# Performance work log

Measured on AMD Instinct MI355X. Metric: run time of the kernel, lower is better.

The kernel has to match this reference:

```python
import jax, jax.numpy as jnp
import numpy as np
import math

TWO_PI = 2.0 * math.pi
LN_EPS = 1e-5


def _phase(pos_f, d):
    # periods[i, j] = i * d + j + 2 ; phi[s, i, j] = cos(2*pi*k_s / periods[i, j])
    i = jnp.arange(d, dtype=jnp.float32)
    periods = i[:, None] * d + i[None, :] + 2.0  # (d, d)
    return jnp.cos(TWO_PI * pos_f[:, None, None] / periods)  # (S, d, d)


def _layernorm(x, g, b):
    mu = jnp.mean(x, axis=-1, keepdims=True)
    var = jnp.mean(jnp.square(x - mu), axis=-1, keepdims=True)
    return (x - mu) * jax.lax.rsqrt(var + LN_EPS) * g + b


def _pos_nk(x, P, phi):
    # Nk[b, s, i] = sum_j P[i, j] * x[b, s, j] * phi[s, i, j]
    return jnp.einsum('bsj,ij,sij->bsi', x, P, phi)


def setup_inputs() -> dict:
    key = jax.random.key(0)
    ks = jax.random.split(key, 10)
    B, S, V, D = 4, 4096, 64, 128
    NTOK = 64  # 4^3 k-mer tokens
    u = lambda k, shp, a: jax.random.uniform(k, shp, jnp.float32, -a, a)
    return {
        'tokens': jax.random.randint(ks[0], (B, S), 0, NTOK, dtype=jnp.int32),
        'positions': jnp.arange(S, dtype=jnp.int32),
        'emb': jax.random.normal(ks[1], (NTOK, V), jnp.float32),
        'char_P': u(ks[2], (V, V), 0.1),
        'M1': u(ks[3], (D, V), 0.5),
        'P1': u(ks[4], (D, D), 0.1),
        'g1': jnp.ones((D,), jnp.float32),
        'b1': jnp.zeros((D,), jnp.float32),
        'R1': u(ks[5], (D, V), 0.1),
        'M2': u(ks[6], (D, D), 0.5),
        'P2': u(ks[7], (D, D), 0.1),
        'g2': jnp.ones((D,), jnp.float32),
        'b2': jnp.zeros((D,), jnp.float32),
    }


def reference(tokens, positions, emb, char_P, M1, P1, g1, b1, R1, M2, P2, g2, b2):
    pos_f = positions.astype(jnp.float32)
    V, D1, D2 = emb.shape[1], M1.shape[0], M2.shape[0]
    # char level (Layer 0): embedding + position-modulated mixing
    x = emb[tokens]                               # (B, S, V)
    h = _pos_nk(x, char_P, _phase(pos_f, V))      # (B, S, V)
    # Layer 1: separate residual (in_dim != out_dim -> linear proj)
    t1 = jnp.einsum('bsj,ij->bsi', h, M1)         # (B, S, D1)
    n1 = _pos_nk(_layernorm(t1, g1, b1), P1, _phase(pos_f, D1))
    h1 = n1 + jnp.einsum('bsj,ij->bsi', h, R1)
    # Layer 2: shared residual (residual = x @ M.T, pre-norm)
    t2 = jnp.einsum('bsj,ij->bsi', h1, M2)        # (B, S, D2)
    n2 = _pos_nk(_layernorm(t2, g2, b2), P2, _phase(pos_f, D2))
    return n2 + t2
```

## Files before the change

kernel.cpp:

```cpp
#include <hip/hip_runtime.h>

typedef unsigned short u16;
typedef unsigned int   u32;
typedef float f32x2 __attribute__((ext_vector_type(2)));

#define BB 4
#define SS 4096
#define VV 64
#define DD 128

#define CPT_OFF 0
#define M1T_OFF 4096
#define R1T_OFF 12288
#define P1T_OFF 20480
#define M2T_OFF 36864
#define P2T_OFF 53248
#define EMB_OFF 69632
#define G1_OFF  73728
#define B1_OFF  73856
#define G2_OFF  73984
#define B2_OFF  74112
#define WS_F32_WEIGHTS 74240

__device__ __forceinline__ float bf2f(u16 u) {
    return __uint_as_float(((u32)u) << 16);
}
__device__ __forceinline__ float ldany(const void* p, int idx, bool f32) {
    return f32 ? ((const float*)p)[idx] : bf2f(((const u16*)p)[idx]);
}
__device__ __forceinline__ float phase_cos(float pos, float pf) {
    float x = pos * __builtin_amdgcn_rcpf(pf);
    float r = __builtin_amdgcn_fractf(x);
    return __builtin_amdgcn_cosf(r);
}
__device__ __forceinline__ float f4get(float4 v, int i) {
    return i == 0 ? v.x : i == 1 ? v.y : i == 2 ? v.z : v.w;
}
struct acc2x2 {
    f32x2 lo, hi;
    __device__ __forceinline__ void zero() { lo = (f32x2)0.f; hi = (f32x2)0.f; }
    __device__ __forceinline__ void fma(float s, float4 v) {
        f32x2 s2 = {s, s};
        f32x2 vlo = {v.x, v.y}, vhi = {v.z, v.w};
        lo = __builtin_elementwise_fma(s2, vlo, lo);
        hi = __builtin_elementwise_fma(s2, vhi, hi);
    }
    __device__ __forceinline__ float get(int b) const {
        return b == 0 ? lo[0] : b == 1 ? lo[1] : b == 2 ? hi[0] : hi[1];
    }
};

__global__ void prep_ws(const void* __restrict__ cP,  const void* __restrict__ M1,
                        const void* __restrict__ R1,  const void* __restrict__ P1,
                        const void* __restrict__ M2,  const void* __restrict__ P2,
                        const void* __restrict__ emb, const void* __restrict__ g1,
                        const void* __restrict__ b1,  const void* __restrict__ g2,
                        const void* __restrict__ b2,  float* __restrict__ wsf)
{
    const bool f32 = (((const u32*)g1)[0] == 0x3F800000u);
    const int m = blockIdx.x;
    const int t = threadIdx.x;
    if (m == 17) {
        for (int idx = t; idx < 4608; idx += 256) {
            float v; int dst;
            if (idx < 4096) { v = ldany(emb, idx, f32); dst = EMB_OFF + idx; }
            else {
                int off = idx - 4096, which = off >> 7, e = off & 127;
                const void* p = (which == 0) ? g1 : (which == 1) ? b1
                              : (which == 2) ? g2 : b2;
                v = ldany(p, e, f32);
                dst = G1_OFF + which * 128 + e;
            }
            wsf[dst] = v;
        }
        return;
    }
    __shared__ float tile[64][65];
    const void* src; int doff, R, C, ti0, tj0;
    if (m == 0)      { src = cP; doff = CPT_OFF; R = 64;  C = 64;  ti0 = 0;            tj0 = 0; }
    else if (m <= 2) { src = M1; doff = M1T_OFF; R = 128; C = 64;  ti0 = (m - 1) * 64; tj0 = 0; }
    else if (m <= 4) { src = R1; doff = R1T_OFF; R = 128; C = 64;  ti0 = (m - 3) * 64; tj0 = 0; }
    else {
        const int k = m - 5, w = k >> 2, q = k & 3;
        src  = (w == 0) ? P1 : (w == 1) ? M2 : P2;
        doff = (w == 0) ? P1T_OFF : (w == 1) ? M2T_OFF : P2T_OFF;
        R = 128; C = 128; ti0 = (q >> 1) * 64; tj0 = (q & 1) * 64;
    }
    float* dst = wsf + doff;
    #pragma unroll
    for (int k = 0; k < 16; ++k) {
        int idx = k * 256 + t;
        int i = idx >> 6, j = idx & 63;
        tile[i][j] = ldany(src, (ti0 + i) * C + (tj0 + j), f32);
    }
    __syncthreads();
    #pragma unroll
    for (int k = 0; k < 16; ++k) {
        int idx = k * 256 + t;
        int j = idx >> 6, i = idx & 63;
        int gj = tj0 + j, gi = ti0 + i;
        dst[((gj >> 2) * R + gi) * 4 + (gj & 3)] = tile[i][j];
    }
}

template<bool WS>
__global__ void __launch_bounds__(256, 4)
fused_hier(const int* __restrict__ tokens,
           const int* __restrict__ positions,
           const void* __restrict__ emb,
           const void* __restrict__ cP,
           const void* __restrict__ M1,
           const void* __restrict__ P1,
           const void* __restrict__ g1,
           const void* __restrict__ b1,
           const void* __restrict__ R1,
           const void* __restrict__ M2,
           const void* __restrict__ P2,
           const void* __restrict__ g2,
           const void* __restrict__ b2,
           const float* __restrict__ wsf,
           float* __restrict__ out)
{
    __shared__ float4 x4v[VV];
    __shared__ float4 h4v[VV];
    __shared__ float4 lnv[DD];
    __shared__ float4 h1v[DD];
    __shared__ float  t14p[4 * DD];
    __shared__ float  t2p[4 * DD];
    __shared__ float  partp[2048];

    float* x4  = (float*)x4v;
    float* h4  = (float*)h4v;
    float* lnf = (float*)lnv;
    float* h1f = (float*)h1v;

    const int t = threadIdx.x;
    const int s = blockIdx.x;
    if (s >= SS) return;
    const bool f32 = WS ? true : (((const u32*)g1)[0] == 0x3F800000u);
    const float pos = (float)positions[s];
    const int i6 = t & 63,  q4 = t >> 6;
    const int i7 = t & 127, h2 = t >> 7;
    const int w  = t >> 6,  l  = t & 63;

    {
        int tok = tokens[q4 * SS + s];
        float v = WS ? wsf[EMB_OFF + tok * VV + i6] : ldany(emb, tok * VV + i6, f32);
        x4[i6 * 4 + q4] = v;
    }
    __syncthreads();

    {
        acc2x2 a; a.zero();
        const int jb = q4 * 16;
        float pf = (float)(i6 * VV + jb + 2);
        #pragma unroll
        for (int q = 0; q < 4; ++q) {
            const int jg = q4 * 4 + q;
            float4 w4;
            if (WS) w4 = *(const float4*)&wsf[CPT_OFF + (jg * VV + i6) * 4];
            #pragma unroll
            for (int k = 0; k < 4; ++k) {
                const int j = jb + q * 4 + k;
                float c  = phase_cos(pos, pf);
                float wt = (WS ? f4get(w4, k) : ldany(cP, i6 * VV + j, f32)) * c;
                a.fma(wt, x4v[j]);
                pf += 1.0f;
            }
        }
        #pragma unroll
        for (int b = 0; b < 4; ++b)
            partp[b * 256 + q4 * 64 + i6] = a.get(b);
    }
    __syncthreads();

    {
        float hv = partp[q4 * 256 + i6]       + partp[q4 * 256 + 64 + i6]
                 + partp[q4 * 256 + 128 + i6] + partp[q4 * 256 + 192 + i6];
        h4[i6 * 4 + q4] = hv;
    }
    __syncthreads();

    {
        acc2x2 at, ar; at.zero(); ar.zero();
        #pragma unroll
        for (int q = 0; q < 8; ++q) {
            const int jg = h2 * 8 + q;
            float4 m4, r4;
            if (WS) {
                m4 = *(const float4*)&wsf[M1T_OFF + (jg * DD + i7) * 4];
                r4 = *(const float4*)&wsf[R1T_OFF + (jg * DD + i7) * 4];
            }
            #pragma unroll
            for (int k = 0; k < 4; ++k) {
                const int j = h2 * 32 + q * 4 + k;
                float mv = WS ? f4get(m4, k) : ldany(M1, i7 * VV + j, f32);
                float rv = WS ? f4get(r4, k) : ldany(R1, i7 * VV + j, f32);
                float4 hb = h4v[j];
                at.fma(mv, hb);
                ar.fma(rv, hb);
            }
        }
        #pragma unroll
        for (int b = 0; b < 4; ++b) {
            partp[b * 256 + h2 * 128 + i7]        = at.get(b);
            partp[1024 + b * 256 + h2 * 128 + i7] = ar.get(b);
        }
    }
    __syncthreads();

    float res0, res1;
    {
        const int b0 = h2 * 2, b1 = b0 + 1;
        t14p[b0 * 128 + i7] = partp[b0 * 256 + i7] + partp[b0 * 256 + 128 + i7];
        t14p[b1 * 128 + i7] = partp[b1 * 256 + i7] + partp[b1 * 256 + 128 + i7];
        res0 = partp[1024 + b0 * 256 + i7] + partp[1024 + b0 * 256 + 128 + i7];
        res1 = partp[1024 + b1 * 256 + i7] + partp[1024 + b1 * 256 + 128 + i7];
    }
    __syncthreads();

    {
        float v0 = t14p[w * 128 + l], v1 = t14p[w * 128 + 64 + l];
        float s1 = v0 + v1;
        #pragma unroll
        for (int m = 1; m < 64; m <<= 1) s1 += __shfl_xor(s1, m, 64);
        float mu = s1 * (1.0f / 128.0f);
        float d0 = v0 - mu, d1 = v1 - mu;
        float s2 = d0 * d0 + d1 * d1;
        #pragma unroll
        for (int m = 1; m < 64; m <<= 1) s2 += __shfl_xor(s2, m, 64);
        float rs = rsqrtf(s2 * (1.0f / 128.0f) + 1e-5f);
        float ga = WS ? wsf[G1_OFF + l]      : ldany(g1, l, f32);
        float gb = WS ? wsf[G1_OFF + l + 64] : ldany(g1, l + 64, f32);
        float ba = WS ? wsf[B1_OFF + l]      : ldany(b1, l, f32);
        float bb = WS ? wsf[B1_OFF + l + 64] : ldany(b1, l + 64, f32);
        lnf[l * 4 + w]        = d0 * rs * ga + ba;
        lnf[(l + 64) * 4 + w] = d1 * rs * gb + bb;
    }
    __syncthreads();

    {
        acc2x2 acc; acc.zero();
        float pf = (float)(i7 * DD + h2 * 64 + 2);
        #pragma unroll
        for (int q = 0; q < 16; ++q) {
            const int jg = h2 * 16 + q;
            float4 w4;
            if (WS) w4 = *(const float4*)&wsf[P1T_OFF + (jg * DD + i7) * 4];
            #pragma unroll
            for (int k = 0; k < 4; ++k) {
                const int j = h2 * 64 + q * 4 + k;
                float c = phase_cos(pos, pf);
                float wt = (WS ? f4get(w4, k) : ldany(P1, i7 * DD + j, f32)) * c;
                acc.fma(wt, lnv[j]);
                pf += 1.0f;
            }
        }
        #pragma unroll
        for (int b = 0; b < 4; ++b)
            partp[b * 256 + h2 * 128 + i7] = acc.get(b);
    }
    __syncthreads();

    {
        const int b0 = h2 * 2, b1 = b0 + 1;
        h1f[i7 * 4 + b0] = res0 + partp[b0 * 256 + i7] + partp[b0 * 256 + 128 + i7];
        h1f[i7 * 4 + b1] = res1 + partp[b1 * 256 + i7] + partp[b1 * 256 + 128 + i7];
    }
    __syncthreads();

    {
        acc2x2 acc; acc.zero();
        #pragma unroll
        for (int q = 0; q < 16; ++q) {
            const int jg = h2 * 16 + q;
            float4 m4;
            if (WS) m4 = *(const float4*)&wsf[M2T_OFF + (jg * DD + i7) * 4];
            #pragma unroll
            for (int k = 0; k < 4; ++k) {
                const int j = h2 * 64 + q * 4 + k;
                float mv = WS ? f4get(m4, k) : ldany(M2, i7 * DD + j, f32);
                acc.fma(mv, h1v[j]);
            }
        }
        #pragma unroll
        for (int b = 0; b < 4; ++b)
            partp[b * 256 + h2 * 128 + i7] = acc.get(b);
    }
    __syncthreads();

    {
        const int b0 = h2 * 2, b1 = b0 + 1;
        t2p[b0 * 128 + i7] = partp[b0 * 256 + i7] + partp[b0 * 256 + 128 + i7];
        t2p[b1 * 128 + i7] = partp[b1 * 256 + i7] + partp[b1 * 256 + 128 + i7];
    }
    __syncthreads();

    {
        float v0 = t2p[w * 128 + l], v1 = t2p[w * 128 + 64 + l];
        float s1 = v0 + v1;
        #pragma unroll
        for (int m = 1; m < 64; m <<= 1) s1 += __shfl_xor(s1, m, 64);
        float mu = s1 * (1.0f / 128.0f);
        float d0 = v0 - mu, d1 = v1 - mu;
        float s2 = d0 * d0 + d1 * d1;
        #pragma unroll
        for (int m = 1; m < 64; m <<= 1) s2 += __shfl_xor(s2, m, 64);
        float rs = rsqrtf(s2 * (1.0f / 128.0f) + 1e-5f);
        float ga = WS ? wsf[G2_OFF + l]      : ldany(g2, l, f32);
        float gb = WS ? wsf[G2_OFF + l + 64] : ldany(g2, l + 64, f32);
        float ba = WS ? wsf[B2_OFF + l]      : ldany(b2, l, f32);
        float bb = WS ? wsf[B2_OFF + l + 64] : ldany(b2, l + 64, f32);
        lnf[l * 4 + w]        = d0 * rs * ga + ba;
        lnf[(l + 64) * 4 + w] = d1 * rs * gb + bb;
    }
    __syncthreads();

    {
        acc2x2 acc; acc.zero();
        float pf = (float)(i7 * DD + h2 * 64 + 2);
        #pragma unroll
        for (int q = 0; q < 16; ++q) {
            const int jg = h2 * 16 + q;
            float4 w4;
            if (WS) w4 = *(const float4*)&wsf[P2T_OFF + (jg * DD + i7) * 4];
            #pragma unroll
            for (int k = 0; k < 4; ++k) {
                const int j = h2 * 64 + q * 4 + k;
                float c = phase_cos(pos, pf);
                float wt = (WS ? f4get(w4, k) : ldany(P2, i7 * DD + j, f32)) * c;
                acc.fma(wt, lnv[j]);
                pf += 1.0f;
            }
        }
        #pragma unroll
        for (int b = 0; b < 4; ++b)
            partp[b * 256 + h2 * 128 + i7] = acc.get(b);
    }
    __syncthreads();

    {
        const int b0 = h2 * 2, b1 = b0 + 1;
        float v0 = partp[b0 * 256 + i7] + partp[b0 * 256 + 128 + i7] + t2p[b0 * 128 + i7];
        float v1 = partp[b1 * 256 + i7] + partp[b1 * 256 + 128 + i7] + t2p[b1 * 128 + i7];
        out[(b0 * SS + s) * DD + i7] = v0;
        out[(b1 * SS + s) * DD + i7] = v1;
    }
}

extern "C" void kernel_launch(void* const* d_in, const int* in_sizes, int n_in,
                              void* d_out, int out_size, void* d_ws, size_t ws_size,
                              hipStream_t stream)
{
    const int* tokens    = (const int*)d_in[0];
    const int* positions = (const int*)d_in[1];
    const void* emb = d_in[2];
    const void* cP  = d_in[3];
    const void* M1  = d_in[4];
    const void* P1  = d_in[5];
    const void* g1  = d_in[6];
    const void* b1  = d_in[7];
    const void* R1  = d_in[8];
    const void* M2  = d_in[9];
    const void* P2  = d_in[10];
    const void* g2  = d_in[11];
    const void* b2  = d_in[12];
    float* out = (float*)d_out;
    float* wsf = (float*)d_ws;

    const bool tw = (ws_size >= (size_t)WS_F32_WEIGHTS * sizeof(float));
    if (tw) {
        prep_ws<<<18, 256, 0, stream>>>(cP, M1, R1, P1, M2, P2, emb,
                                        g1, b1, g2, b2, wsf);
        fused_hier<true><<<SS, 256, 0, stream>>>(tokens, positions, emb, cP, M1, P1,
                                                 g1, b1, R1, M2, P2, g2, b2, wsf, out);
    } else {
        fused_hier<false><<<SS, 256, 0, stream>>>(tokens, positions, emb, cP, M1, P1,
                                                  g1, b1, R1, M2, P2, g2, b2, wsf, out);
    }
}
```

Baseline: 144.8 us.

## Process two sequence positions per block to reuse weight loads and reciprocals

```diff
diff --git a/kernel.cpp b/kernel.cpp
--- a/kernel.cpp
+++ b/kernel.cpp
@@ -28,10 +28,8 @@
 __device__ __forceinline__ float ldany(const void* p, int idx, bool f32) {
     return f32 ? ((const float*)p)[idx] : bf2f(((const u16*)p)[idx]);
 }
-__device__ __forceinline__ float phase_cos(float pos, float pf) {
-    float x = pos * __builtin_amdgcn_rcpf(pf);
-    float r = __builtin_amdgcn_fractf(x);
-    return __builtin_amdgcn_cosf(r);
+__device__ __forceinline__ float cos_rev(float pos, float rcpv) {
+    return __builtin_amdgcn_cosf(__builtin_amdgcn_fractf(pos * rcpv));
 }
 __device__ __forceinline__ float f4get(float4 v, int i) {
     return i == 0 ? v.x : i == 1 ? v.y : i == 2 ? v.z : v.w;
@@ -104,7 +102,7 @@
 }
 
 template<bool WS>
-__global__ void __launch_bounds__(256, 4)
+__global__ void __launch_bounds__(256, 2)
 fused_hier(const int* __restrict__ tokens,
            const int* __restrict__ positions,
            const void* __restrict__ emb,
@@ -121,13 +119,13 @@
            const float* __restrict__ wsf,
            float* __restrict__ out)
 {
-    __shared__ float4 x4v[VV];
-    __shared__ float4 h4v[VV];
-    __shared__ float4 lnv[DD];
-    __shared__ float4 h1v[DD];
-    __shared__ float  t14p[4 * DD];
-    __shared__ float  t2p[4 * DD];
-    __shared__ float  partp[2048];
+    __shared__ float4 x4v[2 * VV];
+    __shared__ float4 h4v[2 * VV];
+    __shared__ float4 lnv[2 * DD];
+    __shared__ float4 h1v[2 * DD];
+    __shared__ float  t14p[2 * 4 * DD];
+    __shared__ float  t2p[2 * 4 * DD];
+    __shared__ float  partp[2 * 2048];
 
     float* x4  = (float*)x4v;
     float* h4  = (float*)h4v;
@@ -135,23 +133,28 @@
     float* h1f = (float*)h1v;
 
     const int t = threadIdx.x;
-    const int s = blockIdx.x;
-    if (s >= SS) return;
+    const int s0 = blockIdx.x;
+    if (s0 >= SS / 2) return;
+    const int s1 = s0 + SS / 2;
     const bool f32 = WS ? true : (((const u32*)g1)[0] == 0x3F800000u);
-    const float pos = (float)positions[s];
+    const float pos0 = (float)positions[s0];
+    const float pos1 = (float)positions[s1];
     const int i6 = t & 63,  q4 = t >> 6;
     const int i7 = t & 127, h2 = t >> 7;
     const int w  = t >> 6,  l  = t & 63;
 
     {
-        int tok = tokens[q4 * SS + s];
-        float v = WS ? wsf[EMB_OFF + tok * VV + i6] : ldany(emb, tok * VV + i6, f32);
-        x4[i6 * 4 + q4] = v;
-    }
-    __syncthreads();
-
-    {
-        acc2x2 a; a.zero();
+        int tk0 = tokens[q4 * SS + s0];
+        int tk1 = tokens[q4 * SS + s1];
+        float v0 = WS ? wsf[EMB_OFF + tk0 * VV + i6] : ldany(emb, tk0 * VV + i6, f32);
+        float v1 = WS ? wsf[EMB_OFF + tk1 * VV + i6] : ldany(emb, tk1 * VV + i6, f32);
+        x4[i6 * 4 + q4]       = v0;
+        x4[256 + i6 * 4 + q4] = v1;
+    }
+    __syncthreads();
+
+    {
+        acc2x2 a0, a1; a0.zero(); a1.zero();
         const int jb = q4 * 16;
         float pf = (float)(i6 * VV + jb + 2);
         #pragma unroll
@@ -162,85 +165,116 @@
             #pragma unroll
             for (int k = 0; k < 4; ++k) {
                 const int j = jb + q * 4 + k;
-                float c  = phase_cos(pos, pf);
-                float wt = (WS ? f4get(w4, k) : ldany(cP, i6 * VV + j, f32)) * c;
-                a.fma(wt, x4v[j]);
+                float rcpv = __builtin_amdgcn_rcpf(pf);
+                float wv = WS ? f4get(w4, k) : ldany(cP, i6 * VV + j, f32);
+                a0.fma(wv * cos_rev(pos0, rcpv), x4v[j]);
+                a1.fma(wv * cos_rev(pos1, rcpv), x4v[64 + j]);
                 pf += 1.0f;
             }
         }
         #pragma unroll
-        for (int b = 0; b < 4; ++b)
-            partp[b * 256 + q4 * 64 + i6] = a.get(b);
-    }
-    __syncthreads();
-
-    {
-        float hv = partp[q4 * 256 + i6]       + partp[q4 * 256 + 64 + i6]
-                 + partp[q4 * 256 + 128 + i6] + partp[q4 * 256 + 192 + i6];
-        h4[i6 * 4 + q4] = hv;
-    }
-    __syncthreads();
-
-    {
-        acc2x2 at, ar; at.zero(); ar.zero();
+        for (int b = 0; b < 4; ++b) {
+            partp[b * 256 + q4 * 64 + i6]        = a0.get(b);
+            partp[2048 + b * 256 + q4 * 64 + i6] = a1.get(b);
+        }
+    }
+    __syncthreads();
+
+    {
+        #pragma unroll
+        for (int p = 0; p < 2; ++p) {
+            const int o = p * 2048;
+            float hv = partp[o + q4 * 256 + i6]       + partp[o + q4 * 256 + 64 + i6]
+                     + partp[o + q4 * 256 + 128 + i6] + partp[o + q4 * 256 + 192 + i6];
+            h4[p * 256 + i6 * 4 + q4] = hv;
+        }
+    }
+    __syncthreads();
+
+    {
+        acc2x2 at0, at1; at0.zero(); at1.zero();
         #pragma unroll
         for (int q = 0; q < 8; ++q) {
             const int jg = h2 * 8 + q;
-            float4 m4, r4;
-            if (WS) {
-                m4 = *(const float4*)&wsf[M1T_OFF + (jg * DD + i7) * 4];
-                r4 = *(const float4*)&wsf[R1T_OFF + (jg * DD + i7) * 4];
-            }
+            float4 m4;
+            if (WS) m4 = *(const float4*)&wsf[M1T_OFF + (jg * DD + i7) * 4];
             #pragma unroll
             for (int k = 0; k < 4; ++k) {
                 const int j = h2 * 32 + q * 4 + k;
                 float mv = WS ? f4get(m4, k) : ldany(M1, i7 * VV + j, f32);
+                at0.fma(mv, h4v[j]);
+                at1.fma(mv, h4v[64 + j]);
+            }
+        }
+        #pragma unroll
+        for (int b = 0; b < 4; ++b) {
+            partp[b * 256 + h2 * 128 + i7]        = at0.get(b);
+            partp[2048 + b * 256 + h2 * 128 + i7] = at1.get(b);
+        }
+    }
+    {
+        acc2x2 ar0, ar1; ar0.zero(); ar1.zero();
+        #pragma unroll
+        for (int q = 0; q < 8; ++q) {
+            const int jg = h2 * 8 + q;
+            float4 r4;
+            if (WS) r4 = *(const float4*)&wsf[R1T_OFF + (jg * DD + i7) * 4];
+            #pragma unroll
+            for (int k = 0; k < 4; ++k) {
+                const int j = h2 * 32 + q * 4 + k;
                 float rv = WS ? f4get(r4, k) : ldany(R1, i7 * VV + j, f32);
-                float4 hb = h4v[j];
-                at.fma(mv, hb);
-                ar.fma(rv, hb);
-            }
-        }
-        #pragma unroll
-        for (int b = 0; b < 4; ++b) {
-            partp[b * 256 + h2 * 128 + i7]        = at.get(b);
-            partp[1024 + b * 256 + h2 * 128 + i7] = ar.get(b);
-        }
-    }
-    __syncthreads();
-
-    float res0, res1;
+                ar0.fma(rv, h4v[j]);
+                ar1.fma(rv, h4v[64 + j]);
+            }
+        }
+        #pragma unroll
+        for (int b = 0; b < 4; ++b) {
+            partp[1024 + b * 256 + h2 * 128 + i7]        = ar0.get(b);
+            partp[2048 + 1024 + b * 256 + h2 * 128 + i7] = ar1.get(b);
+        }
+    }
+    __syncthreads();
+
+    float res[2][2];
     {
         const int b0 = h2 * 2, b1 = b0 + 1;
-        t14p[b0 * 128 + i7] = partp[b0 * 256 + i7] + partp[b0 * 256 + 128 + i7];
-        t14p[b1 * 128 + i7] = partp[b1 * 256 + i7] + partp[b1 * 256 + 128 + i7];
-        res0 = partp[1024 + b0 * 256 + i7] + partp[1024 + b0 * 256 + 128 + i7];
-        res1 = partp[1024 + b1 * 256 + i7] + partp[1024 + b1 * 256 + 128 + i7];
-    }
-    __syncthreads();
-
-    {
-        float v0 = t14p[w * 128 + l], v1 = t14p[w * 128 + 64 + l];
-        float s1 = v0 + v1;
-        #pragma unroll
-        for (int m = 1; m < 64; m <<= 1) s1 += __shfl_xor(s1, m, 64);
-        float mu = s1 * (1.0f / 128.0f);
-        float d0 = v0 - mu, d1 = v1 - mu;
-        float s2 = d0 * d0 + d1 * d1;
-        #pragma unroll
-        for (int m = 1; m < 64; m <<= 1) s2 += __shfl_xor(s2, m, 64);
-        float rs = rsqrtf(s2 * (1.0f / 128.0f) + 1e-5f);
+        #pragma unroll
+        for (int p = 0; p < 2; ++p) {
+            const int o = p * 2048, to = p * 512;
+            t14p[to + b0 * 128 + i7] = partp[o + b0 * 256 + i7] + partp[o + b0 * 256 + 128 + i7];
+            t14p[to + b1 * 128 + i7] = partp[o + b1 * 256 + i7] + partp[o + b1 * 256 + 128 + i7];
+            res[p][0] = partp[o + 1024 + b0 * 256 + i7] + partp[o + 1024 + b0 * 256 + 128 + i7];
+            res[p][1] = partp[o + 1024 + b1 * 256 + i7] + partp[o + 1024 + b1 * 256 + 128 + i7];
+        }
+    }
+    __syncthreads();
+
+    {
         float ga = WS ? wsf[G1_OFF + l]      : ldany(g1, l, f32);
         float gb = WS ? wsf[G1_OFF + l + 64] : ldany(g1, l + 64, f32);
         float ba = WS ? wsf[B1_OFF + l]      : ldany(b1, l, f32);
         float bb = WS ? wsf[B1_OFF + l + 64] : ldany(b1, l + 64, f32);
-        lnf[l * 4 + w]        = d0 * rs * ga + ba;
-        lnf[(l + 64) * 4 + w] = d1 * rs * gb + bb;
-    }
-    __syncthreads();
-
-    {
-        acc2x2 acc; acc.zero();
+        #pragma unroll
+        for (int p = 0; p < 2; ++p) {
+            const int to = p * 512;
+            float v0 = t14p[to + w * 128 + l], v1 = t14p[to + w * 128 + 64 + l];
+            float s1 = v0 + v1;
+            #pragma unroll
+            for (int m = 1; m < 64; m <<= 1) s1 += __shfl_xor(s1, m, 64);
+            float mu = s1 * (1.0f / 128.0f);
+            float d0 = v0 - mu, d1 = v1 - mu;
+            float s2 = d0 * d0 + d1 * d1;
+            #pragma unroll
+            for (int m = 1; m < 64; m <<= 1) s2 += __shfl_xor(s2, m, 64);
+            float rs = rsqrtf(s2 * (1.0f / 128.0f) + 1e-5f);
+            lnf[p * 512 + l * 4 + w]        = d0 * rs * ga + ba;
+            lnf[p * 512 + (l + 64) * 4 + w] = d1 * rs * gb + bb;
+        }
+    }
+    __syncthreads();
+
+    {
+        acc2x2 a0, a1; a0.zero(); a1.zero();
         float pf = (float)(i7 * DD + h2 * 64 + 2);
         #pragma unroll
         for (int q = 0; q < 16; ++q) {
@@ -250,27 +284,34 @@
             #pragma unroll
             for (int k = 0; k < 4; ++k) {
                 const int j = h2 * 64 + q * 4 + k;
-                float c = phase_cos(pos, pf);
-                float wt = (WS ? f4get(w4, k) : ldany(P1, i7 * DD + j, f32)) * c;
-                acc.fma(wt, lnv[j]);
+                float rcpv = __builtin_amdgcn_rcpf(pf);
+                float wv = WS ? f4get(w4, k) : ldany(P1, i7 * DD + j, f32);
+                a0.fma(wv * cos_rev(pos0, rcpv), lnv[j]);
+                a1.fma(wv * cos_rev(pos1, rcpv), lnv[128 + j]);
                 pf += 1.0f;
             }
         }
         #pragma unroll
-        for (int b = 0; b < 4; ++b)
-            partp[b * 256 + h2 * 128 + i7] = acc.get(b);
+        for (int b = 0; b < 4; ++b) {
+            partp[b * 256 + h2 * 128 + i7]        = a0.get(b);
+            partp[2048 + b * 256 + h2 * 128 + i7] = a1.get(b);
+        }
     }
     __syncthreads();
 
     {
         const int b0 = h2 * 2, b1 = b0 + 1;
-        h1f[i7 * 4 + b0] = res0 + partp[b0 * 256 + i7] + partp[b0 * 256 + 128 + i7];
-        h1f[i7 * 4 + b1] = res1 + partp[b1 * 256 + i7] + partp[b1 * 256 + 128 + i7];
-    }
-    __syncthreads();
-
-    {
-        acc2x2 acc; acc.zero();
+        #pragma unroll
+        for (int p = 0; p < 2; ++p) {
+            const int o = p * 2048;
+            h1f[p * 512 + i7 * 4 + b0] = res[p][0] + partp[o + b0 * 256 + i7] + partp[o + b0 * 256 + 128 + i7];
+            h1f[p * 512 + i7 * 4 + b1] = res[p][1] + partp[o + b1 * 256 + i7] + partp[o + b1 * 256 + 128 + i7];
+        }
+    }
+    __syncthreads();
+
+    {
+        acc2x2 a0, a1; a0.zero(); a1.zero();
         #pragma unroll
         for (int q = 0; q < 16; ++q) {
             const int jg = h2 * 16 + q;
@@ -280,44 +321,55 @@
             for (int k = 0; k < 4; ++k) {
                 const int j = h2 * 64 + q * 4 + k;
                 float mv = WS ? f4get(m4, k) : ldany(M2, i7 * DD + j, f32);
-                acc.fma(mv, h1v[j]);
-            }
-        }
-        #pragma unroll
-        for (int b = 0; b < 4; ++b)
-            partp[b * 256 + h2 * 128 + i7] = acc.get(b);
+                a0.fma(mv, h1v[j]);
+                a1.fma(mv, h1v[128 + j]);
+            }
+        }
+        #pragma unroll
+        for (int b = 0; b < 4; ++b) {
+            partp[b * 256 + h2 * 128 + i7]        = a0.get(b);
+            partp[2048 + b * 256 + h2 * 128 + i7] = a1.get(b);
+        }
     }
     __syncthreads();
 
     {
         const int b0 = h2 * 2, b1 = b0 + 1;
-        t2p[b0 * 128 + i7] = partp[b0 * 256 + i7] + partp[b0 * 256 + 128 + i7];
-        t2p[b1 * 128 + i7] = partp[b1 * 256 + i7] + partp[b1 * 256 + 128 + i7];
-    }
-    __syncthreads();
-
-    {
-        float v0 = t2p[w * 128 + l], v1 = t2p[w * 128 + 64 + l];
-        float s1 = v0 + v1;
-        #pragma unroll
-        for (int m = 1; m < 64; m <<= 1) s1 += __shfl_xor(s1, m, 64);
-        float mu = s1 * (1.0f / 128.0f);
-        float d0 = v0 - mu, d1 = v1 - mu;
-        float s2 = d0 * d0 + d1 * d1;
-        #pragma unroll
-        for (int m = 1; m < 64; m <<= 1) s2 += __shfl_xor(s2, m, 64);
-        float rs = rsqrtf(s2 * (1.0f / 128.0f) + 1e-5f);
+        #pragma unroll
+        for (int p = 0; p < 2; ++p) {
+            const int o = p * 2048, to = p * 512;
+            t2p[to + b0 * 128 + i7] = partp[o + b0 * 256 + i7] + partp[o + b0 * 256 + 128 + i7];
+            t2p[to + b1 * 128 + i7] = partp[o + b1 * 256 + i7] + partp[o + b1 * 256 + 128 + i7];
+        }
+    }
+    __syncthreads();
+
+    {
         float ga = WS ? wsf[G2_OFF + l]      : ldany(g2, l, f32);
         float gb = WS ? wsf[G2_OFF + l + 64] : ldany(g2, l + 64, f32);
         float ba = WS ? wsf[B2_OFF + l]      : ldany(b2, l, f32);
         float bb = WS ? wsf[B2_OFF + l + 64] : ldany(b2, l + 64, f32);
-        lnf[l * 4 + w]        = d0 * rs * ga + ba;
-        lnf[(l + 64) * 4 + w] = d1 * rs * gb + bb;
-    }
-    __syncthreads();
-
-    {
-        acc2x2 acc; acc.zero();
+        #pragma unroll
+        for (int p = 0; p < 2; ++p) {
+            const int to = p * 512;
+            float v0 = t2p[to + w * 128 + l], v1 = t2p[to + w * 128 + 64 + l];
+            float s1 = v0 + v1;
+            #pragma unroll
+            for (int m = 1; m < 64; m <<= 1) s1 += __shfl_xor(s1, m, 64);
+            float mu = s1 * (1.0f / 128.0f);
+            float d0 = v0 - mu, d1 = v1 - mu;
+            float s2 = d0 * d0 + d1 * d1;
+            #pragma unroll
+            for (int m = 1; m < 64; m <<= 1) s2 += __shfl_xor(s2, m, 64);
+            float rs = rsqrtf(s2 * (1.0f / 128.0f) + 1e-5f);
+            lnf[p * 512 + l * 4 + w]        = d0 * rs * ga + ba;
+            lnf[p * 512 + (l + 64) * 4 + w] = d1 * rs * gb + bb;
+        }
+    }
+    __syncthreads();
+
+    {
+        acc2x2 a0, a1; a0.zero(); a1.zero();
         float pf = (float)(i7 * DD + h2 * 64 + 2);
         #pragma unroll
         for (int q = 0; q < 16; ++q) {
@@ -327,24 +379,32 @@
             #pragma unroll
             for (int k = 0; k < 4; ++k) {
                 const int j = h2 * 64 + q * 4 + k;
-                float c = phase_cos(pos, pf);
-                float wt = (WS ? f4get(w4, k) : ldany(P2, i7 * DD + j, f32)) * c;
-                acc.fma(wt, lnv[j]);
+                float rcpv = __builtin_amdgcn_rcpf(pf);
+                float wv = WS ? f4get(w4, k) : ldany(P2, i7 * DD + j, f32);
+                a0.fma(wv * cos_rev(pos0, rcpv), lnv[j]);
+                a1.fma(wv * cos_rev(pos1, rcpv), lnv[128 + j]);
                 pf += 1.0f;
             }
         }
         #pragma unroll
-        for (int b = 0; b < 4; ++b)
-            partp[b * 256 + h2 * 128 + i7] = acc.get(b);
+        for (int b = 0; b < 4; ++b) {
+            partp[b * 256 + h2 * 128 + i7]        = a0.get(b);
+            partp[2048 + b * 256 + h2 * 128 + i7] = a1.get(b);
+        }
     }
     __syncthreads();
 
     {
         const int b0 = h2 * 2, b1 = b0 + 1;
-        float v0 = partp[b0 * 256 + i7] + partp[b0 * 256 + 128 + i7] + t2p[b0 * 128 + i7];
-        float v1 = partp[b1 * 256 + i7] + partp[b1 * 256 + 128 + i7] + t2p[b1 * 128 + i7];
-        out[(b0 * SS + s) * DD + i7] = v0;
-        out[(b1 * SS + s) * DD + i7] = v1;
+        #pragma unroll
+        for (int p = 0; p < 2; ++p) {
+            const int o = p * 2048, to = p * 512;
+            const int sp = p == 0 ? s0 : s1;
+            float v0 = partp[o + b0 * 256 + i7] + partp[o + b0 * 256 + 128 + i7] + t2p[to + b0 * 128 + i7];
+            float v1 = partp[o + b1 * 256 + i7] + partp[o + b1 * 256 + 128 + i7] + t2p[to + b1 * 128 + i7];
+            out[(b0 * SS + sp) * DD + i7] = v0;
+            out[(b1 * SS + sp) * DD + i7] = v1;
+        }
     }
 }
 
@@ -372,10 +432,10 @@
     if (tw) {
         prep_ws<<<18, 256, 0, stream>>>(cP, M1, R1, P1, M2, P2, emb,
                                         g1, b1, g2, b2, wsf);
-        fused_hier<true><<<SS, 256, 0, stream>>>(tokens, positions, emb, cP, M1, P1,
-                                                 g1, b1, R1, M2, P2, g2, b2, wsf, out);
+        fused_hier<true><<<SS / 2, 256, 0, stream>>>(tokens, positions, emb, cP, M1, P1,
+                                                     g1, b1, R1, M2, P2, g2, b2, wsf, out);
     } else {
-        fused_hier<false><<<SS, 256, 0, stream>>>(tokens, positions, emb, cP, M1, P1,
-                                                  g1, b1, R1, M2, P2, g2, b2, wsf, out);
-    }
-}
+        fused_hier<false><<<SS / 2, 256, 0, stream>>>(tokens, positions, emb, cP, M1, P1,
+                                                      g1, b1, R1, M2, P2, g2, b2, wsf, out);
+    }
+}
```

Measured after the change: 148.0 us. +2.2%, slower.

## Replace shared-memory split-K partial reductions with intra-wave shuffle reductions

Applied to the files above, without the earlier changes.

```diff
diff --git a/kernel.cpp b/kernel.cpp
--- a/kernel.cpp
+++ b/kernel.cpp
@@ -47,6 +47,12 @@
     }
     __device__ __forceinline__ float get(int b) const {
         return b == 0 ? lo[0] : b == 1 ? lo[1] : b == 2 ? hi[0] : hi[1];
+    }
+    __device__ __forceinline__ void red_xor(int m) {
+        lo[0] += __shfl_xor(lo[0], m, 64);
+        lo[1] += __shfl_xor(lo[1], m, 64);
+        hi[0] += __shfl_xor(hi[0], m, 64);
+        hi[1] += __shfl_xor(hi[1], m, 64);
     }
 };
 
@@ -127,7 +133,6 @@
     __shared__ float4 h1v[DD];
     __shared__ float  t14p[4 * DD];
     __shared__ float  t2p[4 * DD];
-    __shared__ float  partp[2048];
 
     float* x4  = (float*)x4v;
     float* h4  = (float*)h4v;
@@ -139,24 +144,28 @@
     if (s >= SS) return;
     const bool f32 = WS ? true : (((const u32*)g1)[0] == 0x3F800000u);
     const float pos = (float)positions[s];
-    const int i6 = t & 63,  q4 = t >> 6;
-    const int i7 = t & 127, h2 = t >> 7;
-    const int w  = t >> 6,  l  = t & 63;
-
-    {
-        int tok = tokens[q4 * SS + s];
-        float v = WS ? wsf[EMB_OFF + tok * VV + i6] : ldany(emb, tok * VV + i6, f32);
-        x4[i6 * 4 + q4] = v;
+    const int wv = t >> 6, L = t & 63;
+    const int i7 = wv * 32 + (L & 31);
+    const int jh = L >> 5;
+    const int i6 = wv * 16 + (L & 15);
+    const int jq = (L >> 4) & 3;
+    const int w  = wv, l = L;
+
+    {
+        int tok = tokens[wv * SS + s];
+        int ie  = t & 63;
+        float v = WS ? wsf[EMB_OFF + tok * VV + ie] : ldany(emb, tok * VV + ie, f32);
+        x4[ie * 4 + wv] = v;
     }
     __syncthreads();
 
     {
         acc2x2 a; a.zero();
-        const int jb = q4 * 16;
+        const int jb = jq * 16;
         float pf = (float)(i6 * VV + jb + 2);
         #pragma unroll
         for (int q = 0; q < 4; ++q) {
-            const int jg = q4 * 4 + q;
+            const int jg = jq * 4 + q;
             float4 w4;
             if (WS) w4 = *(const float4*)&wsf[CPT_OFF + (jg * VV + i6) * 4];
             #pragma unroll
@@ -168,24 +177,18 @@
                 pf += 1.0f;
             }
         }
-        #pragma unroll
-        for (int b = 0; b < 4; ++b)
-            partp[b * 256 + q4 * 64 + i6] = a.get(b);
-    }
-    __syncthreads();
-
-    {
-        float hv = partp[q4 * 256 + i6]       + partp[q4 * 256 + 64 + i6]
-                 + partp[q4 * 256 + 128 + i6] + partp[q4 * 256 + 192 + i6];
-        h4[i6 * 4 + q4] = hv;
-    }
-    __syncthreads();
-
+        a.red_xor(16);
+        a.red_xor(32);
+        h4[i6 * 4 + jq] = a.get(jq);
+    }
+    __syncthreads();
+
+    float resv0, resv1;
     {
         acc2x2 at, ar; at.zero(); ar.zero();
         #pragma unroll
         for (int q = 0; q < 8; ++q) {
-            const int jg = h2 * 8 + q;
+            const int jg = jh * 8 + q;
             float4 m4, r4;
             if (WS) {
                 m4 = *(const float4*)&wsf[M1T_OFF + (jg * DD + i7) * 4];
@@ -193,7 +196,7 @@
             }
             #pragma unroll
             for (int k = 0; k < 4; ++k) {
-                const int j = h2 * 32 + q * 4 + k;
+                const int j = jh * 32 + q * 4 + k;
                 float mv = WS ? f4get(m4, k) : ldany(M1, i7 * VV + j, f32);
                 float rv = WS ? f4get(r4, k) : ldany(R1, i7 * VV + j, f32);
                 float4 hb = h4v[j];
@@ -201,21 +204,13 @@
                 ar.fma(rv, hb);
             }
         }
-        #pragma unroll
-        for (int b = 0; b < 4; ++b) {
-            partp[b * 256 + h2 * 128 + i7]        = at.get(b);
-            partp[1024 + b * 256 + h2 * 128 + i7] = ar.get(b);
-        }
-    }
-    __syncthreads();
-
-    float res0, res1;
-    {
-        const int b0 = h2 * 2, b1 = b0 + 1;
-        t14p[b0 * 128 + i7] = partp[b0 * 256 + i7] + partp[b0 * 256 + 128 + i7];
-        t14p[b1 * 128 + i7] = partp[b1 * 256 + i7] + partp[b1 * 256 + 128 + i7];
-        res0 = partp[1024 + b0 * 256 + i7] + partp[1024 + b0 * 256 + 128 + i7];
-        res1 = partp[1024 + b1 * 256 + i7] + partp[1024 + b1 * 256 + 128 + i7];
+        at.red_xor(32);
+        ar.red_xor(32);
+        const int b0 = jh * 2, b1 = b0 + 1;
+        t14p[b0 * 128 + i7] = at.get(b0);
+        t14p[b1 * 128 + i7] = at.get(b1);
+        resv0 = ar.get(b0);
+        resv1 = ar.get(b1);
     }
     __syncthreads();
 
@@ -241,58 +236,49 @@
 
     {
         acc2x2 acc; acc.zero();
-        float pf = (float)(i7 * DD + h2 * 64 + 2);
+        float pf = (float)(i7 * DD + jh * 64 + 2);
         #pragma unroll
         for (int q = 0; q < 16; ++q) {
-            const int jg = h2 * 16 + q;
+            const int jg = jh * 16 + q;
             float4 w4;
             if (WS) w4 = *(const float4*)&wsf[P1T_OFF + (jg * DD + i7) * 4];
             #pragma unroll
             for (int k = 0; k < 4; ++k) {
-                const int j = h2 * 64 + q * 4 + k;
+                const int j = jh * 64 + q * 4 + k;
                 float c = phase_cos(pos, pf);
                 float wt = (WS ? f4get(w4, k) : ldany(P1, i7 * DD + j, f32)) * c;
                 acc.fma(wt, lnv[j]);
                 pf += 1.0f;
             }
         }
-        #pragma unroll
-        for (int b = 0; b < 4; ++b)
-            partp[b * 256 + h2 * 128 + i7] = acc.get(b);
-    }
-    __syncthreads();
-
-    {
-        const int b0 = h2 * 2, b1 = b0 + 1;
-        h1f[i7 * 4 + b0] = res0 + partp[b0 * 256 + i7] + partp[b0 * 256 + 128 + i7];
-        h1f[i7 * 4 + b1] = res1 + partp[b1 * 256 + i7] + partp[b1 * 256 + 128 + i7];
-    }
-    __syncthreads();
-
+        acc.red_xor(32);
+        const int b0 = jh * 2, b1 = b0 + 1;
+        h1f[i7 * 4 + b0] = resv0 + acc.get(b0);
+        h1f[i7 * 4 + b1] = resv1 + acc.get(b1);
+    }
+    __syncthreads();
+
+    float t2v0, t2v1;
     {
         acc2x2 acc; acc.zero();
         #pragma unroll
         for (int q = 0; q < 16; ++q) {
-            const int jg = h2 * 16 + q;
+            const int jg = jh * 16 + q;
             float4 m4;
             if (WS) m4 = *(const float4*)&wsf[M2T_OFF + (jg * DD + i7) * 4];
             #pragma unroll
             for (int k = 0; k < 4; ++k) {
-                const int j = h2 * 64 + q * 4 + k;
+                const int j = jh * 64 + q * 4 + k;
                 float mv = WS ? f4get(m4, k) : ldany(M2, i7 * DD + j, f32);
                 acc.fma(mv, h1v[j]);
             }
         }
-        #pragma unroll
-        for (int b = 0; b < 4; ++b)
-            partp[b * 256 + h2 * 128 + i7] = acc.get(b);
-    }
-    __syncthreads();
-
-    {
-        const int b0 = h2 * 2, b1 = b0 + 1;
-        t2p[b0 * 128 + i7] = partp[b0 * 256 + i7] + partp[b0 * 256 + 128 + i7];
-        t2p[b1 * 128 + i7] = partp[b1 * 256 + i7] + partp[b1 * 256 + 128 + i7];
+        acc.red_xor(32);
+        const int b0 = jh * 2, b1 = b0 + 1;
+        t2p[b0 * 128 + i7] = acc.get(b0);
+        t2p[b1 * 128 + i7] = acc.get(b1);
+        t2v0 = acc.get(b0);
+        t2v1 = acc.get(b1);
     }
     __syncthreads();
 
@@ -318,33 +304,25 @@
 
     {
         acc2x2 acc; acc.zero();
-        float pf = (float)(i7 * DD + h2 * 64 + 2);
+        float pf = (float)(i7 * DD + jh * 64 + 2);
         #pragma unroll
         for (int q = 0; q < 16; ++q) {
-            const int jg = h2 * 16 + q;
+            const int jg = jh * 16 + q;
             float4 w4;
             if (WS) w4 = *(const float4*)&wsf[P2T_OFF + (jg * DD + i7) * 4];
             #pragma unroll
             for (int k = 0; k < 4; ++k) {
-                const int j = h2 * 64 + q * 4 + k;
+                const int j = jh * 64 + q * 4 + k;
                 float c = phase_cos(pos, pf);
                 float wt = (WS ? f4get(w4, k) : ldany(P2, i7 * DD + j, f32)) * c;
                 acc.fma(wt, lnv[j]);
                 pf += 1.0f;
             }
         }
-        #pragma unroll
-        for (int b = 0; b < 4; ++b)
-            partp[b * 256 + h2 * 128 + i7] = acc.get(b);
-    }
-    __syncthreads();
-
-    {
-        const int b0 = h2 * 2, b1 = b0 + 1;
-        float v0 = partp[b0 * 256 + i7] + partp[b0 * 256 + 128 + i7] + t2p[b0 * 128 + i7];
-        float v1 = partp[b1 * 256 + i7] + partp[b1 * 256 + 128 + i7] + t2p[b1 * 128 + i7];
-        out[(b0 * SS + s) * DD + i7] = v0;
-        out[(b1 * SS + s) * DD + i7] = v1;
+        acc.red_xor(32);
+        const int b0 = jh * 2, b1 = b0 + 1;
+        out[(b0 * SS + s) * DD + i7] = acc.get(b0) + t2v0;
+        out[(b1 * SS + s) * DD + i7] = acc.get(b1) + t2v1;
     }
 }
 
```

Result: no change. 144.4 us (-0.3%).
